# Performance work log

Hardware: AMD Instinct MI355X
Metric: run time of the kernel (lower is better)

## Reference

```python
import jax, jax.numpy as jnp
import numpy as np

DIM = 768
H = 12
HD = 64  # head_dim = dim // num_heads
SCALE = HD ** (-0.5)
EPS = 1e-6


def setup_inputs() -> dict:
    key = jax.random.key(0)
    k1, k2, k3, k4, k5 = jax.random.split(key, 5)
    B, N = 8, 1024
    x = jax.random.normal(k1, (B, N, DIM), dtype=jnp.float32)
    policy = jax.random.uniform(k2, (B, N, 1), dtype=jnp.float32)
    # nn.Linear weights: [out_features, in_features]; qkv_bias=False, proj has bias
    qkv_w = jax.random.normal(k3, (3 * H * HD, DIM), dtype=jnp.float32) * (DIM ** -0.5)
    proj_w = jax.random.normal(k4, (DIM, H * HD), dtype=jnp.float32) * ((H * HD) ** -0.5)
    proj_b = jax.random.normal(k5, (DIM,), dtype=jnp.float32) * 0.01
    return {"x": x, "policy": policy, "qkv_w": qkv_w, "proj_w": proj_w, "proj_b": proj_b}


def _softmax_with_policy(attn, policy):
    # attn: [B,H,N,N], policy: [B,N,1]
    B, Hh, N, _ = attn.shape
    attn_policy = policy.reshape(B, 1, 1, N)
    eye = jnp.eye(N, dtype=attn_policy.dtype).reshape(1, 1, N, N)
    attn_policy = attn_policy + (1.0 - attn_policy) * eye
    max_att = jnp.max(attn, axis=-1, keepdims=True)
    a = jnp.exp((attn - max_att).astype(jnp.float32)) * attn_policy.astype(jnp.float32)
    a = (a + EPS / N) / (jnp.sum(a, axis=-1, keepdims=True) + EPS)
    return a.astype(max_att.dtype)


def reference(x, policy, qkv_w, proj_w, proj_b):
    B, N, C = x.shape
    qkv = (x @ qkv_w.T).reshape(B, N, 3, H, HD)
    qkv = jnp.transpose(qkv, (2, 0, 3, 1, 4))  # [3,B,H,N,HD]
    q, k, v = qkv[0], qkv[1], qkv[2]
    attn = jnp.einsum('bhnd,bhmd->bhnm', q * SCALE, k)  # [B,H,N,N]
    attn = _softmax_with_policy(attn, policy)
    out = jnp.einsum('bhnm,bhmd->bhnd', attn, v)  # [B,H,N,HD]
    out = jnp.transpose(out, (0, 2, 1, 3)).reshape(B, N, H * HD)
    return out @ proj_w.T + proj_b
```

## Files before the change

### kernel.cpp

```cpp
#include <hip/hip_runtime.h>

typedef __bf16 bf16x8 __attribute__((ext_vector_type(8)));
typedef float floatx4 __attribute__((ext_vector_type(4)));

#define EPSF 1e-6f

__device__ inline unsigned short f2bf(float f) {
  union { float f; unsigned u; } x; x.f = f;
  unsigned r = x.u + 0x7FFFu + ((x.u >> 16) & 1u);
  return (unsigned short)(r >> 16);
}
__device__ inline float bf2f(unsigned short u) {
  union { unsigned u; float f; } x; x.u = ((unsigned)u) << 16;
  return x.f;
}
__device__ inline unsigned pk2bf(float lo, float hi) {
  union { float f; unsigned u; } a, b; a.f = lo; b.f = hi;
  unsigned ua = a.u + 0x8000u, ub = b.u + 0x8000u;
  return (ub & 0xFFFF0000u) | (ua >> 16);
}

__device__ inline floatx4 mfma16(bf16x8 a, bf16x8 b, floatx4 c) {
  return __builtin_amdgcn_mfma_f32_16x16x32_bf16(a, b, c, 0, 0, 0);
}

__device__ inline void gll16(const unsigned short* g, unsigned short* l) {
  __builtin_amdgcn_global_load_lds((__attribute__((address_space(1))) void*)g,
                                   (__attribute__((address_space(3))) void*)l, 16, 0, 0);
}

__global__ __launch_bounds__(256) void prep_kernel(const float* __restrict__ x,
                                                   const float* __restrict__ qkv_w,
                                                   const float* __restrict__ proj_w,
                                                   const float* __restrict__ policy,
                                                   unsigned short* __restrict__ xb,
                                                   unsigned short* __restrict__ wqkv,
                                                   unsigned short* __restrict__ wproj,
                                                   unsigned short* __restrict__ pbf) {
  const int bid = blockIdx.x, tid = threadIdx.x;
  if (bid < 3072) {
    const int i = bid * 2048 + tid * 8;
    float4 v0 = *(const float4*)(x + i);
    float4 v1 = *(const float4*)(x + i + 4);
    __align__(16) unsigned short o[8] = {f2bf(v0.x), f2bf(v0.y), f2bf(v0.z), f2bf(v0.w),
                                         f2bf(v1.x), f2bf(v1.y), f2bf(v1.z), f2bf(v1.w)};
    *(float4*)(xb + i) = *(float4*)o;
  } else if (bid < 3936) {
    const int i = (bid - 3072) * 2048 + tid * 8;
    const float s = (i < 589824) ? 0.18033688011112042f : 1.0f;
    float4 v0 = *(const float4*)(qkv_w + i);
    float4 v1 = *(const float4*)(qkv_w + i + 4);
    __align__(16) unsigned short o[8] = {
        f2bf(v0.x * s), f2bf(v0.y * s), f2bf(v0.z * s), f2bf(v0.w * s),
        f2bf(v1.x * s), f2bf(v1.y * s), f2bf(v1.z * s), f2bf(v1.w * s)};
    *(float4*)(wqkv + i) = *(float4*)o;
  } else if (bid < 4224) {
    const int i0 = (bid - 3936) * 2048 + tid * 8;
    const int base = (i0 / 768) * 768 + ((i0 % 768) & ~63);
    __align__(16) unsigned short o[8];
#pragma unroll
    for (int t = 0; t < 8; t++) {
      const int cp = (i0 + t) & 63;
      const int c = 16 * (cp & 3) + (cp >> 2);
      o[t] = f2bf(proj_w[base + c]);
    }
    *(float4*)(wproj + i0) = *(float4*)o;
  } else {
    const int idx = (bid - 4224) * 256 + tid;
    const int b = idx >> 10, g = idx & 1023;
    const int chunk = g >> 5, w = g & 31;
    const int c = (chunk << 5) + (w >> 1) + ((w & 1) << 4);
    pbf[idx] = f2bf(policy[b * 1024 + c]);
  }
}

template <int EP, int BN>
__global__ __launch_bounds__(256, 3) void gemm_bt(const unsigned short* __restrict__ A,
                                                  const unsigned short* __restrict__ Bt,
                                                  void* __restrict__ Cout,
                                                  const float* __restrict__ bias,
                                                  int M, int N, int K) {
  constexpr int J = BN / 32;
  __shared__ __align__(16) unsigned short sA[128 * 64];
  __shared__ __align__(16) unsigned short sB[BN * 64];
  const int m0 = blockIdx.y * 128, n0 = blockIdx.x * BN;
  const int tid = threadIdx.x;
  const int lane = tid & 63, wave = tid >> 6;
  const int qd = lane >> 4, l15 = lane & 15;
  const int wr = (wave >> 1) * 64, wc = (wave & 1) * (BN / 2);
  const int srow = tid >> 3;
  const int scb = (tid & 7) ^ (srow & 7);
  const unsigned short* Ag = A + (long)(m0 + srow) * K + scb * 8;
  const unsigned short* Bg = Bt + (long)(n0 + srow) * K + scb * 8;
  const int x7 = l15 & 7;
  floatx4 acc[4][J] = {};
  for (int k0 = 0; k0 < K; k0 += 64) {
    __syncthreads();
#pragma unroll
    for (int p = 0; p < 4; p++) gll16(Ag + (long)(p * 32) * K + k0, sA + p * 2048 + wave * 512);
#pragma unroll
    for (int p = 0; p < J; p++) gll16(Bg + (long)(p * 32) * K + k0, sB + p * 2048 + wave * 512);
    __syncthreads();
#pragma unroll
    for (int s = 0; s < 2; s++) {
      const int cw = ((s * 4 + qd) ^ x7) * 8;
      bf16x8 af[4], bf[J];
#pragma unroll
      for (int i = 0; i < 4; i++) af[i] = *(const bf16x8*)&sA[(wr + i * 16 + l15) * 64 + cw];
#pragma unroll
      for (int j = 0; j < J; j++) bf[j] = *(const bf16x8*)&sB[(wc + j * 16 + l15) * 64 + cw];
#pragma unroll
      for (int i = 0; i < 4; i++)
#pragma unroll
        for (int j = 0; j < J; j++) acc[i][j] = mfma16(af[i], bf[j], acc[i][j]);
    }
  }
  if constexpr (EP == 0) {
#pragma unroll
    for (int i = 0; i < 4; i++)
#pragma unroll
      for (int r = 0; r < 4; r++) {
        const int row = m0 + wr + i * 16 + qd * 4 + r;
        __align__(8) unsigned short pk[4];
#pragma unroll
        for (int j = 0; j < 4; j++) pk[j] = f2bf(acc[i][j][r]);
        *(uint2*)((unsigned short*)Cout + (long)row * N + n0 + wc + 4 * l15) = *(uint2*)pk;
      }
  } else {
#pragma unroll
    for (int i = 0; i < 4; i++)
#pragma unroll
      for (int j = 0; j < J; j++) {
        const int col = n0 + wc + j * 16 + l15;
#pragma unroll
        for (int r = 0; r < 4; r++) {
          const int row = m0 + wr + i * 16 + qd * 4 + r;
          ((float*)Cout)[(long)row * N + col] = acc[i][j][r] + bias[col];
        }
      }
  }
}

__global__ __launch_bounds__(256) void transpose_v(const unsigned short* __restrict__ qkv,
                                                   const float* __restrict__ policy,
                                                   unsigned short* __restrict__ vTp) {
  __shared__ unsigned short tile[64][72];
  __shared__ float sPol[64];
  const int bh = blockIdx.y;
  const int b = bh / 12, h = bh % 12;
  const int n0 = blockIdx.x * 64;
  const int t = threadIdx.x;
  if (t < 64) sPol[t] = policy[b * 1024 + n0 + t];
  {
    const int nr = t >> 2, dc = (t & 3) * 16;
    const unsigned short* src = qkv + (long)(b * 1024 + n0 + nr) * 2304 + 2 * 768 + h * 64 + dc;
    float4 v0 = *(const float4*)src;
    float4 v1 = *(const float4*)(src + 8);
    *(float4*)&tile[nr][dc] = v0;
    *(float4*)&tile[nr][dc + 8] = v1;
  }
  __syncthreads();
  {
    const int d = t >> 2, nc = (t & 3) * 16;
    __align__(16) unsigned short o[16];
#pragma unroll
    for (int jj = 0; jj < 16; jj++) {
      const int cc = nc + jj;
      const int w = cc & 31;
      const int cl = (cc & 32) + (w >> 1) + ((w & 1) << 4);
      o[jj] = f2bf(bf2f(tile[cl][d]) * sPol[cl]);
    }
    unsigned short* dst = vTp + (long)(bh * 64 + d) * 1024 + n0 + nc;
    *(float4*)dst = *(float4*)&o[0];
    *(float4*)(dst + 8) = *(float4*)&o[8];
  }
}

__global__ __launch_bounds__(256, 3) void attn_kernel(const unsigned short* __restrict__ qkv,
                                                      const unsigned short* __restrict__ vTp,
                                                      const unsigned short* __restrict__ pbf,
                                                      const float* __restrict__ policy,
                                                      unsigned short* __restrict__ aout) {
  __shared__ __align__(16) unsigned short sK[2][2048];
  __shared__ __align__(16) unsigned short sV[2][2048];
  __shared__ __align__(16) unsigned short sP[4][2][2][640];
  __shared__ __align__(16) unsigned short sPv[1024];
  __shared__ float sD[4][32];
  const int bid = blockIdx.x;
  const int bh = bid % 96, qt = bid / 96;
  const int b = bh / 12, h = bh % 12;
  const int tid = threadIdx.x;
  const int wave = tid >> 6, lane = tid & 63;
  const int qd = lane >> 4, l15 = lane & 15;
  const int q0 = qt * 128 + wave * 32;
  const unsigned short* qb = qkv + (long)(b * 1024 + q0 + l15) * 2304 + h * 64 + qd * 8;
  bf16x8 qf00 = *(const bf16x8*)qb;
  bf16x8 qf01 = *(const bf16x8*)(qb + 32);
  bf16x8 qf10 = *(const bf16x8*)(qb + (long)16 * 2304);
  bf16x8 qf11 = *(const bf16x8*)(qb + (long)16 * 2304 + 32);
  if (tid < 128) *(float4*)(sPv + tid * 8) = *(const float4*)(pbf + b * 1024 + tid * 8);
  const int krow = wave * 8 + (lane >> 3);
  const int kcb = (lane & 7) ^ (lane >> 3);
  const unsigned short* kgl = qkv + (long)(b * 1024 + krow) * 2304 + 768 + h * 64 + kcb * 8;
  const int vrow = tid >> 2;
  const int vcb = (tid & 3) ^ ((vrow ^ (vrow >> 2)) & 3);
  const unsigned short* vgl = vTp + (long)(bh * 64 + vrow) * 1024 + vcb * 8;
  const int x7 = l15 & 7;
  const int vsw = (qd ^ ((l15 ^ (l15 >> 2)) & 3)) * 8;
  floatx4 O0[4] = {}, O1[4] = {};
  floatx4 Dl0 = {}, Dl1 = {};
  gll16(kgl, &sK[0][wave * 512]);
  gll16(vgl, &sV[0][wave * 512]);
  __builtin_amdgcn_s_waitcnt(0);
  __syncthreads();
  for (int it = 0; it < 32; ++it) {
    const int buf = it & 1;
    if (it < 31) {
      gll16(kgl + (long)(32 * (it + 1)) * 2304, &sK[buf ^ 1][wave * 512]);
      gll16(vgl + 32 * (it + 1), &sV[buf ^ 1][wave * 512]);
    }
    const int c0 = it * 32;
    bf16x8 k00 = *(const bf16x8*)&sK[buf][(0 * 16 + l15) * 64 + ((0 * 4 + qd) ^ x7) * 8];
    bf16x8 k01 = *(const bf16x8*)&sK[buf][(0 * 16 + l15) * 64 + ((1 * 4 + qd) ^ x7) * 8];
    bf16x8 k10 = *(const bf16x8*)&sK[buf][(1 * 16 + l15) * 64 + ((0 * 4 + qd) ^ x7) * 8];
    bf16x8 k11 = *(const bf16x8*)&sK[buf][(1 * 16 + l15) * 64 + ((1 * 4 + qd) ^ x7) * 8];
    bf16x8 pv = *(const bf16x8*)&sPv[c0 + qd * 8];
    floatx4 z = {0.f, 0.f, 0.f, 0.f};
    floatx4 s00 = mfma16(qf01, k01, mfma16(qf00, k00, z));
    floatx4 s01 = mfma16(qf01, k11, mfma16(qf00, k10, z));
    floatx4 s10 = mfma16(qf11, k01, mfma16(qf10, k00, z));
    floatx4 s11 = mfma16(qf11, k11, mfma16(qf10, k10, z));
    unsigned short* w0 = &sP[wave][buf][0][0];
    unsigned short* w1 = &sP[wave][buf][1][0];
#pragma unroll
    for (int r = 0; r < 4; r++) {
      const int row = qd * 4 + r;
      ((unsigned*)w0)[row * 20 + l15] = pk2bf(exp2f(s00[r]), exp2f(s01[r]));
      ((unsigned*)w1)[row * 20 + l15] = pk2bf(exp2f(s10[r]), exp2f(s11[r]));
    }
    bf16x8 pf0 = *(const bf16x8*)&w0[l15 * 40 + qd * 8];
    bf16x8 pf1 = *(const bf16x8*)&w1[l15 * 40 + qd * 8];
    bf16x8 vf0 = *(const bf16x8*)&sV[buf][(0 * 16 + l15) * 32 + vsw];
    bf16x8 vf1 = *(const bf16x8*)&sV[buf][(1 * 16 + l15) * 32 + vsw];
    bf16x8 vf2 = *(const bf16x8*)&sV[buf][(2 * 16 + l15) * 32 + vsw];
    bf16x8 vf3 = *(const bf16x8*)&sV[buf][(3 * 16 + l15) * 32 + vsw];
    Dl0 = mfma16(pf0, pv, Dl0);
    Dl1 = mfma16(pf1, pv, Dl1);
    O0[0] = mfma16(pf0, vf0, O0[0]); O1[0] = mfma16(pf1, vf0, O1[0]);
    O0[1] = mfma16(pf0, vf1, O0[1]); O1[1] = mfma16(pf1, vf1, O1[1]);
    O0[2] = mfma16(pf0, vf2, O0[2]); O1[2] = mfma16(pf1, vf2, O1[2]);
    O0[3] = mfma16(pf0, vf3, O0[3]); O1[3] = mfma16(pf1, vf3, O1[3]);
    __builtin_amdgcn_s_waitcnt(0);
    __syncthreads();
  }
  {
    const unsigned short* kd = qkv + (long)(b * 1024 + q0 + l15) * 2304 + 768 + h * 64 + qd * 8;
    bf16x8 kd00 = *(const bf16x8*)kd;
    bf16x8 kd01 = *(const bf16x8*)(kd + 32);
    bf16x8 kd10 = *(const bf16x8*)(kd + (long)16 * 2304);
    bf16x8 kd11 = *(const bf16x8*)(kd + (long)16 * 2304 + 32);
    float part0 = 0.f, part1 = 0.f;
#pragma unroll
    for (int jj = 0; jj < 8; jj++) {
      part0 += (float)qf00[jj] * (float)kd00[jj] + (float)qf01[jj] * (float)kd01[jj];
      part1 += (float)qf10[jj] * (float)kd10[jj] + (float)qf11[jj] * (float)kd11[jj];
    }
    part0 += __shfl_xor(part0, 16); part0 += __shfl_xor(part0, 32);
    part1 += __shfl_xor(part1, 16); part1 += __shfl_xor(part1, 32);
    const float p0 = policy[b * 1024 + q0 + l15];
    const float p1 = policy[b * 1024 + q0 + 16 + l15];
    if (qd == 0) {
      sD[wave][l15] = exp2f(part0) * (1.0f - p0);
      sD[wave][16 + l15] = exp2f(part1) * (1.0f - p1);
    }
    __builtin_amdgcn_s_waitcnt(0);
    const unsigned short* vdiag = qkv + (long)(b * 1024 + q0) * 2304 + 1536 + h * 64 + l15;
#pragma unroll
    for (int r = 0; r < 4; r++) {
      const int row = qd * 4 + r;
      const float c0v = sD[wave][row], c1v = sD[wave][16 + row];
#pragma unroll
      for (int j = 0; j < 4; j++) {
        O0[j][r] += c0v * bf2f(vdiag[(long)row * 2304 + j * 16]);
        O1[j][r] += c1v * bf2f(vdiag[(long)(16 + row) * 2304 + j * 16]);
      }
      Dl0[r] += c0v;
      Dl1[r] += c1v;
    }
  }
  const long ob = (long)(b * 1024 + q0 + qd * 4) * 768 + h * 64 + l15;
#pragma unroll
  for (int r = 0; r < 4; r++) {
    const float li0 = 1.0f / (Dl0[r] + EPSF);
    const float li1 = 1.0f / (Dl1[r] + EPSF);
#pragma unroll
    for (int j = 0; j < 4; j++) {
      aout[ob + (long)r * 768 + j * 16] = f2bf(O0[j][r] * li0);
      aout[ob + (long)(16 * 768) + r * 768 + j * 16] = f2bf(O1[j][r] * li1);
    }
  }
}

extern "C" void kernel_launch(void* const* d_in, const int* in_sizes, int n_in,
                              void* d_out, int out_size, void* d_ws, size_t ws_size,
                              hipStream_t stream) {
  const float* x      = (const float*)d_in[0];
  const float* policy = (const float*)d_in[1];
  const float* qkv_w  = (const float*)d_in[2];
  const float* proj_w = (const float*)d_in[3];
  const float* proj_b = (const float*)d_in[4];
  float* out = (float*)d_out;

  char* ws = (char*)d_ws;
  unsigned short* xb    = (unsigned short*)(ws + 0);
  unsigned short* wqkv  = (unsigned short*)(ws + 12582912);
  unsigned short* wproj = (unsigned short*)(ws + 16121856);
  unsigned short* qkvb  = (unsigned short*)(ws + 17301504);
  unsigned short* vTp   = (unsigned short*)(ws + 55050240);
  unsigned short* aoutb = (unsigned short*)(ws + 67633152);
  unsigned short* pbf   = (unsigned short*)(ws + 80216064);

  prep_kernel<<<4256, 256, 0, stream>>>(x, qkv_w, proj_w, policy, xb, wqkv, wproj, pbf);
  gemm_bt<0, 128><<<dim3(18, 64), 256, 0, stream>>>(xb, wqkv, qkvb, nullptr, 8192, 2304, 768);
  transpose_v<<<dim3(16, 96), 256, 0, stream>>>(qkvb, policy, vTp);
  attn_kernel<<<dim3(768), 256, 0, stream>>>(qkvb, vTp, pbf, policy, aoutb);
  gemm_bt<1, 64><<<dim3(12, 64), 256, 0, stream>>>(aoutb, wproj, out, proj_b, 8192, 768, 768);
}
```

Before: 199.9 us.

## Compute transposed QK^T so softmax probabilities stay in registers for PV MFMA

Swaps the operand order of the QK^T MFMAs so each lane's accumulator outputs already match the operand layout the PV MFMA expects, removing the per-iteration LDS round trip through the sP buffer. The key-column permutation is changed to a new sigma_inv mapping, applied consistently to the policy bf16 vector and the transposed, policy-scaled V. This eliminates LDS writes and reads plus the LDS footprint, at the cost of an extra permutation in the prep kernels.

```diff
diff --git a/kernel.cpp b/kernel.cpp
--- a/kernel.cpp
+++ b/kernel.cpp
@@ -27,6 +27,11 @@
 __device__ inline void gll16(const unsigned short* g, unsigned short* l) {
   __builtin_amdgcn_global_load_lds((__attribute__((address_space(1))) void*)g,
                                    (__attribute__((address_space(3))) void*)l, 16, 0, 0);
+}
+
+__device__ __host__ inline int sigma_inv(int p) {
+  const int qq = p >> 3, jj = p & 7;
+  return (jj < 4) ? (qq * 4 + jj) : (16 + qq * 4 + jj - 4);
 }
 
 __global__ __launch_bounds__(256) void prep_kernel(const float* __restrict__ x,
@@ -68,8 +73,7 @@
   } else {
     const int idx = (bid - 4224) * 256 + tid;
     const int b = idx >> 10, g = idx & 1023;
-    const int chunk = g >> 5, w = g & 31;
-    const int c = (chunk << 5) + (w >> 1) + ((w & 1) << 4);
+    const int c = ((g >> 5) << 5) + sigma_inv(g & 31);
     pbf[idx] = f2bf(policy[b * 1024 + c]);
   }
 }
@@ -166,8 +170,7 @@
 #pragma unroll
     for (int jj = 0; jj < 16; jj++) {
       const int cc = nc + jj;
-      const int w = cc & 31;
-      const int cl = (cc & 32) + (w >> 1) + ((w & 1) << 4);
+      const int cl = (cc & 32) + sigma_inv(cc & 31);
       o[jj] = f2bf(bf2f(tile[cl][d]) * sPol[cl]);
     }
     unsigned short* dst = vTp + (long)(bh * 64 + d) * 1024 + n0 + nc;
@@ -183,7 +186,6 @@
                                                       unsigned short* __restrict__ aout) {
   __shared__ __align__(16) unsigned short sK[2][2048];
   __shared__ __align__(16) unsigned short sV[2][2048];
-  __shared__ __align__(16) unsigned short sP[4][2][2][640];
   __shared__ __align__(16) unsigned short sPv[1024];
   __shared__ float sD[4][32];
   const int bid = blockIdx.x;
@@ -220,26 +222,27 @@
       gll16(vgl + 32 * (it + 1), &sV[buf ^ 1][wave * 512]);
     }
     const int c0 = it * 32;
-    bf16x8 k00 = *(const bf16x8*)&sK[buf][(0 * 16 + l15) * 64 + ((0 * 4 + qd) ^ x7) * 8];
-    bf16x8 k01 = *(const bf16x8*)&sK[buf][(0 * 16 + l15) * 64 + ((1 * 4 + qd) ^ x7) * 8];
-    bf16x8 k10 = *(const bf16x8*)&sK[buf][(1 * 16 + l15) * 64 + ((0 * 4 + qd) ^ x7) * 8];
-    bf16x8 k11 = *(const bf16x8*)&sK[buf][(1 * 16 + l15) * 64 + ((1 * 4 + qd) ^ x7) * 8];
+    bf16x8 k00 = *(const bf16x8*)&sK[buf][(0 * 16 + l15) * 64 + ((0 + qd) ^ x7) * 8];
+    bf16x8 k01 = *(const bf16x8*)&sK[buf][(0 * 16 + l15) * 64 + ((4 + qd) ^ x7) * 8];
+    bf16x8 k10 = *(const bf16x8*)&sK[buf][(1 * 16 + l15) * 64 + ((0 + qd) ^ x7) * 8];
+    bf16x8 k11 = *(const bf16x8*)&sK[buf][(1 * 16 + l15) * 64 + ((4 + qd) ^ x7) * 8];
     bf16x8 pv = *(const bf16x8*)&sPv[c0 + qd * 8];
     floatx4 z = {0.f, 0.f, 0.f, 0.f};
-    floatx4 s00 = mfma16(qf01, k01, mfma16(qf00, k00, z));
-    floatx4 s01 = mfma16(qf01, k11, mfma16(qf00, k10, z));
-    floatx4 s10 = mfma16(qf11, k01, mfma16(qf10, k00, z));
-    floatx4 s11 = mfma16(qf11, k11, mfma16(qf10, k10, z));
-    unsigned short* w0 = &sP[wave][buf][0][0];
-    unsigned short* w1 = &sP[wave][buf][1][0];
-#pragma unroll
-    for (int r = 0; r < 4; r++) {
-      const int row = qd * 4 + r;
-      ((unsigned*)w0)[row * 20 + l15] = pk2bf(exp2f(s00[r]), exp2f(s01[r]));
-      ((unsigned*)w1)[row * 20 + l15] = pk2bf(exp2f(s10[r]), exp2f(s11[r]));
-    }
-    bf16x8 pf0 = *(const bf16x8*)&w0[l15 * 40 + qd * 8];
-    bf16x8 pf1 = *(const bf16x8*)&w1[l15 * 40 + qd * 8];
+    floatx4 tA0 = mfma16(k01, qf01, mfma16(k00, qf00, z));
+    floatx4 tB0 = mfma16(k11, qf01, mfma16(k10, qf00, z));
+    floatx4 tA1 = mfma16(k01, qf11, mfma16(k00, qf10, z));
+    floatx4 tB1 = mfma16(k11, qf11, mfma16(k10, qf10, z));
+    uint4 pu0, pu1;
+    pu0.x = pk2bf(exp2f(tA0[0]), exp2f(tA0[1]));
+    pu0.y = pk2bf(exp2f(tA0[2]), exp2f(tA0[3]));
+    pu0.z = pk2bf(exp2f(tB0[0]), exp2f(tB0[1]));
+    pu0.w = pk2bf(exp2f(tB0[2]), exp2f(tB0[3]));
+    pu1.x = pk2bf(exp2f(tA1[0]), exp2f(tA1[1]));
+    pu1.y = pk2bf(exp2f(tA1[2]), exp2f(tA1[3]));
+    pu1.z = pk2bf(exp2f(tB1[0]), exp2f(tB1[1]));
+    pu1.w = pk2bf(exp2f(tB1[2]), exp2f(tB1[3]));
+    bf16x8 pf0 = *(bf16x8*)&pu0;
+    bf16x8 pf1 = *(bf16x8*)&pu1;
     bf16x8 vf0 = *(const bf16x8*)&sV[buf][(0 * 16 + l15) * 32 + vsw];
     bf16x8 vf1 = *(const bf16x8*)&sV[buf][(1 * 16 + l15) * 32 + vsw];
     bf16x8 vf2 = *(const bf16x8*)&sV[buf][(2 * 16 + l15) * 32 + vsw];
```

Measured after the change: 203.6 us. Within noise of the previous version (+1.8%).
